# Performance work log

Hardware: AMD Instinct MI355X
Metric: run time of the kernel (lower is better)

Reference implementation:

```python
import jax, jax.numpy as jnp
import numpy as np

E, H, L = 512, 512, 1   # emb_size, hidden_size, num_layers
B, S, T = 64, 1024, 256  # batch, src_len, trg_len
SCALE = 0.02


def setup_inputs() -> dict:
    key = jax.random.key(0)
    ks = jax.random.split(key, 12)
    f32 = jnp.float32
    return {
        # forward args
        "trg_embed": jax.random.normal(ks[0], (B, T, E), f32),
        "encoder_hidden": jax.random.normal(ks[1], (B, S, 2 * H), f32),
        "encoder_final": jax.random.normal(ks[2], (L, B, 2 * H), f32),
        "src_mask": jnp.ones((B, 1, S), jnp.bool_),
        "trg_mask": jnp.ones((B, 1, T), jnp.bool_),
        # Bahdanau attention params
        "W_key": jax.random.normal(ks[3], (H, 2 * H), f32) * SCALE,
        "W_query": jax.random.normal(ks[4], (H, H), f32) * SCALE,
        "v_energy": jax.random.normal(ks[5], (H,), f32) * SCALE,
        # bridge (2H -> H, with bias)
        "W_bridge": jax.random.normal(ks[6], (H, 2 * H), f32) * SCALE,
        "b_bridge": jnp.zeros((H,), f32),
        # GRU (single layer), gate order r,z,n as in torch
        "W_ih": jax.random.normal(ks[7], (3 * H, E + 2 * H), f32) * SCALE,
        "W_hh": jax.random.normal(ks[8], (3 * H, H), f32) * SCALE,
        "b_ih": jnp.zeros((3 * H,), f32),
        "b_hh": jnp.zeros((3 * H,), f32),
        # pre_output_layer: (H + 2H + E) -> H, no bias
        "W_pre": jax.random.normal(ks[9], (H, H + 2 * H + E), f32) * SCALE,
    }


def _gru_cell(x, h, W_ih, W_hh, b_ih, b_hh):
    # x: [B, E+2H], h: [B, H]; torch GRUCell math, gates r,z,n
    gi = x @ W_ih.T + b_ih
    gh = h @ W_hh.T + b_hh
    i_r, i_z, i_n = jnp.split(gi, 3, axis=-1)
    h_r, h_z, h_n = jnp.split(gh, 3, axis=-1)
    r = jax.nn.sigmoid(i_r + h_r)
    z = jax.nn.sigmoid(i_z + h_z)
    n = jnp.tanh(i_n + r * h_n)
    return (1.0 - z) * n + z * h


def reference(trg_embed, encoder_hidden, encoder_final, src_mask, trg_mask,
              W_key, W_query, v_energy, W_bridge, b_bridge,
              W_ih, W_hh, b_ih, b_hh, W_pre):
    # init_hidden: tanh(bridge(encoder_final))  -> [L, B, H]
    hidden0 = jnp.tanh(jnp.einsum('lbd,hd->lbh', encoder_final, W_bridge) + b_bridge)
    # precomputed attention keys: [B, S, H]
    proj_key = jnp.einsum('bsd,hd->bsh', encoder_hidden, W_key)
    mask = src_mask[:, 0, :]  # [B, S]
    neg = jnp.finfo(trg_embed.dtype).min

    def step(hidden, prev_embed):  # hidden [L,B,H], prev_embed [B,E]
        q = hidden[-1] @ W_query.T                       # [B, H]
        e = jnp.tanh(q[:, None, :] + proj_key)           # [B, S, H]
        scores = jnp.einsum('bsh,h->bs', e, v_energy)    # [B, S]
        scores = jnp.where(mask, scores, neg)
        alphas = jax.nn.softmax(scores, axis=-1)         # [B, S]
        context = jnp.einsum('bs,bsd->bd', alphas, encoder_hidden)  # [B, 2H]
        x = jnp.concatenate([prev_embed, context], axis=-1)         # [B, E+2H]
        h_new = _gru_cell(x, hidden[-1], W_ih, W_hh, b_ih, b_hh)    # [B, H]
        pre = jnp.concatenate([prev_embed, h_new, context], axis=-1) @ W_pre.T  # [B, H]
        return h_new[None, :, :], (h_new, pre)

    hidden_final, (outs, pres) = jax.lax.scan(step, hidden0, jnp.swapaxes(trg_embed, 0, 1))
    decoder_states = jnp.swapaxes(outs, 0, 1)        # [B, T, H]
    pre_output_vectors = jnp.swapaxes(pres, 0, 1)    # [B, T, H]
    return decoder_states, hidden_final, pre_output_vectors
```

## Files before the change

### kernel.cpp

```cpp
#include <hip/hip_runtime.h>


typedef __attribute__((ext_vector_type(8))) short bf16x8;
typedef __attribute__((ext_vector_type(4))) float f32x4;
typedef __attribute__((ext_vector_type(2))) float f32x2;
typedef unsigned short u16;
typedef unsigned char u8;
typedef unsigned int u32;

constexpr int NB = 64, NS = 1024, NT = 256, NE = 512, NH = 512, NH2 = 1024, NG3 = 1536;

#define MFMA16(a, b, c) __builtin_amdgcn_mfma_f32_16x16x32_bf16((a), (b), (c), 0, 0, 0)

__device__ __forceinline__ float bf2f(u16 u) { return __uint_as_float(((u32)u) << 16); }
__device__ __forceinline__ u16 f2bf(float f) {
    u32 u = __float_as_uint(f);
    u += 0x7FFFu + ((u >> 16) & 1u);
    return (u16)(u >> 16);
}
__device__ __forceinline__ float fast_tanh(float x) {
    float t = __expf(2.0f * x);
    return 1.0f - __fdividef(2.0f, t + 1.0f);
}
__device__ __forceinline__ float fast_sig(float x) {
    return __fdividef(1.0f, 1.0f + __expf(-x));
}

__global__ void k_cast(const float* __restrict__ src, u16* __restrict__ dst, int n4) {
    int i = blockIdx.x * blockDim.x + threadIdx.x;
    int stride = gridDim.x * blockDim.x;
    for (; i < n4; i += stride) {
        float4 v = reinterpret_cast<const float4*>(src)[i];
        ushort4 o;
        o.x = f2bf(v.x); o.y = f2bf(v.y); o.z = f2bf(v.z); o.w = f2bf(v.w);
        reinterpret_cast<ushort4*>(dst)[i] = o;
    }
}
__global__ void k_cast8(const float* __restrict__ src, u32* __restrict__ dst, int n8) {
    int i = blockIdx.x * blockDim.x + threadIdx.x;
    int stride = gridDim.x * blockDim.x;
    for (; i < n8; i += stride) {
        float4 a = reinterpret_cast<const float4*>(src)[i * 2];
        float4 b = reinterpret_cast<const float4*>(src)[i * 2 + 1];
        int w0 = 0, w1 = 0;
        w0 = __builtin_amdgcn_cvt_pk_fp8_f32(a.x, a.y, w0, false);
        w0 = __builtin_amdgcn_cvt_pk_fp8_f32(a.z, a.w, w0, true);
        w1 = __builtin_amdgcn_cvt_pk_fp8_f32(b.x, b.y, w1, false);
        w1 = __builtin_amdgcn_cvt_pk_fp8_f32(b.z, b.w, w1, true);
        uint2 o; o.x = (u32)w0; o.y = (u32)w1;
        reinterpret_cast<uint2*>(dst)[i] = o;
    }
}

__global__ __launch_bounds__(256) void k_pkgemm8(
    const float* __restrict__ A, const u16* __restrict__ Bm, u8* __restrict__ Out8) {
    __shared__ u16 As[128][72];
    __shared__ u16 Bs[128][72];
    const int mt = blockIdx.x, nt = blockIdx.y;
    const int tid = threadIdx.x, lane = tid & 63, wv = tid >> 6;
    const int m0 = mt * 128, n0 = nt * 128;
    const f32x4 fz = {0.f, 0.f, 0.f, 0.f};
    f32x4 acc[2][8];
#pragma unroll
    for (int i = 0; i < 2; ++i)
#pragma unroll
        for (int jj = 0; jj < 8; ++jj) acc[i][jj] = fz;

    for (int kt = 0; kt < 16; ++kt) {
        const int k0 = kt * 64;
        __syncthreads();
#pragma unroll
        for (int r = 0; r < 4; ++r) {
            int cc = tid + 256 * r;
            int row = cc >> 3, kc = (cc & 7) * 8;
            const float* ap = &A[(size_t)(m0 + row) * NH2 + k0 + kc];
            float4 f0 = *(const float4*)ap;
            float4 f1 = *(const float4*)(ap + 4);
            u16 hh[8] = {f2bf(f0.x), f2bf(f0.y), f2bf(f0.z), f2bf(f0.w),
                         f2bf(f1.x), f2bf(f1.y), f2bf(f1.z), f2bf(f1.w)};
            *(bf16x8*)&As[row][kc] = *(bf16x8*)hh;
            *(bf16x8*)&Bs[row][kc] = *(const bf16x8*)&Bm[(size_t)(n0 + row) * NH2 + k0 + kc];
        }
        __syncthreads();
#pragma unroll
        for (int ks = 0; ks < 2; ++ks) {
            const int kk = ks * 32 + (lane >> 4) * 8;
            bf16x8 a0 = *(const bf16x8*)&As[wv * 32 + (lane & 15)][kk];
            bf16x8 a1 = *(const bf16x8*)&As[wv * 32 + 16 + (lane & 15)][kk];
#pragma unroll
            for (int jj = 0; jj < 8; ++jj) {
                bf16x8 bb = *(const bf16x8*)&Bs[jj * 16 + (lane & 15)][kk];
                acc[0][jj] = MFMA16(a0, bb, acc[0][jj]);
                acc[1][jj] = MFMA16(a1, bb, acc[1][jj]);
            }
        }
    }
#pragma unroll
    for (int i = 0; i < 2; ++i)
#pragma unroll
        for (int jj = 0; jj < 8; ++jj)
#pragma unroll
            for (int r = 0; r < 4; ++r) {
                int m = m0 + wv * 32 + i * 16 + (lane >> 4) * 4 + r;
                int n = n0 + jj * 16 + (lane & 15);
                int pk = __builtin_amdgcn_cvt_pk_fp8_f32(acc[i][jj][r], acc[i][jj][r], 0, false);
                Out8[(size_t)m * NH + n] = (u8)(pk & 0xFF);
            }
}

__global__ __launch_bounds__(256) void k_bridge(
    const float* __restrict__ ef, const float* __restrict__ Wb, const float* __restrict__ bb,
    float* __restrict__ hf, u16* __restrict__ hbb) {
    __shared__ float efs[NH2];
    const int b = blockIdx.x, tid = threadIdx.x;
    for (int i = tid; i < NH2; i += 256) efs[i] = ef[(size_t)b * NH2 + i];
    __syncthreads();
    for (int j = tid; j < NH; j += 256) {
        float acc = bb[j];
        const float4* wr = (const float4*)&Wb[(size_t)j * NH2];
#pragma unroll 4
        for (int d4 = 0; d4 < 256; ++d4) {
            float4 w = wr[d4];
            acc += w.x * efs[d4 * 4] + w.y * efs[d4 * 4 + 1] + w.z * efs[d4 * 4 + 2] + w.w * efs[d4 * 4 + 3];
        }
        float h0 = tanhf(acc);
        hf[(size_t)b * NH + j] = h0;
        hbb[(size_t)b * NH + j] = f2bf(h0);
    }
}

__global__ __launch_bounds__(256, 4) void k_attn(
    const u8* __restrict__ pk8, const u8* __restrict__ eh8,
    const float* __restrict__ qb, const float* __restrict__ ven,
    u16* __restrict__ ctxp, float* __restrict__ denp) {
    __shared__ float wts[64];
    __shared__ float wden[4];
    __shared__ float part[64][4][17];
    const int b = blockIdx.x >> 4, c = blockIdx.x & 15;
    const int tid = threadIdx.x, lane = tid & 63, wv = tid >> 6;
    const int sl = lane & 3, ch = lane >> 2;
    const int h0 = ch * 32;
    const float C = 2.8853900817779268f;
    float qv2[32], vvm2[32];
    float vs = 0.f;
#pragma unroll
    for (int i4 = 0; i4 < 8; ++i4) {
        float4 q4 = *(const float4*)&qb[(size_t)b * NH + h0 + i4 * 4];
        float4 v4 = *(const float4*)&ven[h0 + i4 * 4];
        qv2[i4 * 4 + 0] = C * q4.x; qv2[i4 * 4 + 1] = C * q4.y;
        qv2[i4 * 4 + 2] = C * q4.z; qv2[i4 * 4 + 3] = C * q4.w;
        vvm2[i4 * 4 + 0] = -2.f * v4.x; vvm2[i4 * 4 + 1] = -2.f * v4.y;
        vvm2[i4 * 4 + 2] = -2.f * v4.z; vvm2[i4 * 4 + 3] = -2.f * v4.w;
        vs += v4.x + v4.y + v4.z + v4.w;
    }
#pragma unroll
    for (int off = 32; off; off >>= 1) vs += __shfl_xor(vs, off, 64);
    vs *= 0.25f;

    const u8* pkbase = pk8 + ((size_t)b * NS + c * 64 + wv * 16 + sl) * NH + h0;
    u32 pk[4][8];
#pragma unroll
    for (int g = 0; g < 4; ++g) {
        const u8* row = pkbase + (size_t)g * 4 * NH;
        *(uint4*)&pk[g][0] = *(const uint4*)row;
        *(uint4*)&pk[g][4] = *(const uint4*)(row + 16);
    }
    float accg[4];
#pragma unroll
    for (int g = 0; g < 4; ++g) {
        float acc0 = 0.f, acc1 = 0.f;
#pragma unroll
        for (int w = 0; w < 8; ++w) {
            f32x2 lo = __builtin_amdgcn_cvt_pk_f32_fp8(pk[g][w], false);
            f32x2 hi = __builtin_amdgcn_cvt_pk_f32_fp8(pk[g][w], true);
            const int i = w * 4;
            float x0 = __builtin_fmaf(lo[0], C, qv2[i + 0]);
            float x1 = __builtin_fmaf(lo[1], C, qv2[i + 1]);
            float x2 = __builtin_fmaf(hi[0], C, qv2[i + 2]);
            float x3 = __builtin_fmaf(hi[1], C, qv2[i + 3]);
            acc0 = __builtin_fmaf(vvm2[i + 0], __builtin_amdgcn_rcpf(__builtin_amdgcn_exp2f(x0) + 1.0f), acc0);
            acc1 = __builtin_fmaf(vvm2[i + 1], __builtin_amdgcn_rcpf(__builtin_amdgcn_exp2f(x1) + 1.0f), acc1);
            acc0 = __builtin_fmaf(vvm2[i + 2], __builtin_amdgcn_rcpf(__builtin_amdgcn_exp2f(x2) + 1.0f), acc0);
            acc1 = __builtin_fmaf(vvm2[i + 3], __builtin_amdgcn_rcpf(__builtin_amdgcn_exp2f(x3) + 1.0f), acc1);
        }
        accg[g] = acc0 + acc1;
    }
#pragma unroll
    for (int off = 4; off <= 32; off <<= 1) {
#pragma unroll
        for (int g = 0; g < 4; ++g) accg[g] += __shfl_xor(accg[g], off, 64);
    }
    float den_acc = 0.f;
#pragma unroll
    for (int g = 0; g < 4; ++g) {
        float w = __expf(accg[g] + vs);
        if (lane < 4) wts[wv * 16 + g * 4 + lane] = w;
        den_acc += w;
    }
#pragma unroll
    for (int off = 32; off; off >>= 1) den_acc += __shfl_xor(den_acc, off, 64);
    if (lane == 0) wden[wv] = den_acc * 0.0625f;

    const int qd = wv, tt = lane;
    const int d0 = tt * 16;
    const u8* ebase = eh8 + ((size_t)b * NS + c * 64 + qd * 16) * NH2 + d0;
    float ar[16];
#pragma unroll
    for (int k = 0; k < 16; ++k) ar[k] = 0.f;
#pragma unroll 4
    for (int s = 0; s < 16; ++s) {
        float w = wts[qd * 16 + s];
        uint4 uu = *(const uint4*)&ebase[(size_t)s * NH2];
        const u32 ww[4] = {uu.x, uu.y, uu.z, uu.w};
#pragma unroll
        for (int q = 0; q < 4; ++q) {
            f32x2 plo = __builtin_amdgcn_cvt_pk_f32_fp8(ww[q], false);
            f32x2 phi = __builtin_amdgcn_cvt_pk_f32_fp8(ww[q], true);
            ar[q * 4 + 0] = __builtin_fmaf(w, plo[0], ar[q * 4 + 0]);
            ar[q * 4 + 1] = __builtin_fmaf(w, plo[1], ar[q * 4 + 1]);
            ar[q * 4 + 2] = __builtin_fmaf(w, phi[0], ar[q * 4 + 2]);
            ar[q * 4 + 3] = __builtin_fmaf(w, phi[1], ar[q * 4 + 3]);
        }
    }
#pragma unroll
    for (int k = 0; k < 16; ++k) part[tt][qd][k] = ar[k];
    __syncthreads();
    if (tid == 0) denp[c * 64 + b] = wden[0] + wden[1] + wden[2] + wden[3];
    const int st = tid >> 2, k0 = (tid & 3) * 4;
    float o0 = 0.f, o1 = 0.f, o2 = 0.f, o3 = 0.f;
#pragma unroll
    for (int q = 0; q < 4; ++q) {
        o0 += part[st][q][k0 + 0];
        o1 += part[st][q][k0 + 1];
        o2 += part[st][q][k0 + 2];
        o3 += part[st][q][k0 + 3];
    }
    ushort4 o;
    o.x = f2bf(o0); o.y = f2bf(o1); o.z = f2bf(o2); o.w = f2bf(o3);
    *(ushort4*)&ctxp[((size_t)c * 64 + b) * NH2 + tid * 4] = o;
}

__global__ __launch_bounds__(256) void k_norm(
    const u16* __restrict__ ctxp, const float* __restrict__ denp,
    u16* __restrict__ ctxb, u16* __restrict__ ctxall, int t) {
    const int b = blockIdx.x >> 1, half = blockIdx.x & 1;
    const int tid = threadIdx.x;
    float den = 0.f;
#pragma unroll
    for (int c = 0; c < 16; ++c) den += denp[c * 64 + b];
    float rd = 1.0f / den;
    const int d0 = half * 512 + tid * 2;
    float ax = 0.f, ay = 0.f;
#pragma unroll
    for (int c = 0; c < 16; ++c) {
        ushort2 v = *(const ushort2*)&ctxp[((size_t)c * 64 + b) * NH2 + d0];
        ax += bf2f(v.x); ay += bf2f(v.y);
    }
    ushort2 o;
    o.x = f2bf(ax * rd); o.y = f2bf(ay * rd);
    *(ushort2*)&ctxb[(size_t)b * NH2 + d0] = o;
    *(ushort2*)&ctxall[((size_t)b * NT + t) * NH2 + d0] = o;
}

__global__ __launch_bounds__(512) void k_gru(
    const u16* __restrict__ teb, const u16* __restrict__ ctxb, const u16* __restrict__ hb_in,
    const u16* __restrict__ Wihb, const u16* __restrict__ Whhb,
    const float* __restrict__ bih, const float* __restrict__ bhh,
    const float* __restrict__ hf_in, float* __restrict__ hf_out, u16* __restrict__ hb_out,
    u16* __restrict__ hall, float* __restrict__ out_ds, float* __restrict__ out_hf, int t) {
    __shared__ float pbuf[3][7][16][17];
    const int tid = threadIdx.x, lane = tid & 63, wv = tid >> 6;
    const int g = blockIdx.x;
    const int jt = g & 31, mh = g >> 5;
    const int jj = lane & 15;
    const int j = jt * 16 + jj;
    const int kg = lane >> 4;
    const int mrow = mh * 8 + (jj & 7);

    const f32x4 fz = {0.f, 0.f, 0.f, 0.f};
    f32x4 g0 = fz, g1 = fz, g2 = fz;
    const u16* wr = Wihb + (size_t)j * NG3;
    const u16* wz = wr + (size_t)NH * NG3;
    const u16* wn = wr + (size_t)NH2 * NG3;
    float ho[4], bset[6];

    if (wv < 2) {
        const u16* ta = teb + ((size_t)mrow * NT + t) * NE;
#pragma unroll
        for (int kt = 0; kt < 8; ++kt) {
            int k0 = (wv * 8 + kt) * 32 + kg * 8;
            bf16x8 a = *(const bf16x8*)&ta[k0];
            g0 = MFMA16(a, *(const bf16x8*)&wr[k0], g0);
            g1 = MFMA16(a, *(const bf16x8*)&wz[k0], g1);
            g2 = MFMA16(a, *(const bf16x8*)&wn[k0], g2);
        }
        if (wv == 0) {
            bset[0] = bih[j]; bset[1] = bih[NH + j]; bset[2] = bih[NH2 + j];
            bset[3] = bhh[j]; bset[4] = bhh[NH + j]; bset[5] = bhh[NH2 + j];
#pragma unroll
            for (int r = 0; r < 4; ++r) {
                int ml = kg * 4 + r;
                ho[r] = (ml < 8) ? hf_in[(size_t)(mh * 8 + ml) * NH + j] : 0.f;
            }
        }
    } else if (wv < 4) {
        const u16* ha = hb_in + (size_t)mrow * NH;
        const u16* vr = Whhb + (size_t)j * NH;
        const u16* vz = vr + (size_t)NH * NH;
        const u16* vn = vr + (size_t)NH2 * NH;
#pragma unroll
        for (int kt = 0; kt < 8; ++kt) {
            int k0 = ((wv - 2) * 8 + kt) * 32 + kg * 8;
            bf16x8 a = *(const bf16x8*)&ha[k0];
            g0 = MFMA16(a, *(const bf16x8*)&vr[k0], g0);
            g1 = MFMA16(a, *(const bf16x8*)&vz[k0], g1);
            g2 = MFMA16(a, *(const bf16x8*)&vn[k0], g2);
        }
    } else {
        const int koff = (wv - 4) * 256;
        const u16* ca = ctxb + (size_t)mrow * NH2;
#pragma unroll
        for (int kt = 0; kt < 8; ++kt) {
            int kc = koff + kt * 32 + kg * 8;
            bf16x8 a = *(const bf16x8*)&ca[kc];
            g0 = MFMA16(a, *(const bf16x8*)&wr[NE + kc], g0);
            g1 = MFMA16(a, *(const bf16x8*)&wz[NE + kc], g1);
            g2 = MFMA16(a, *(const bf16x8*)&wn[NE + kc], g2);
        }
    }
    if (wv != 0) {
        const int src = wv - 1;
#pragma unroll
        for (int r = 0; r < 4; ++r) {
            int ml = kg * 4 + r;
            pbuf[0][src][ml][jj] = g0[r];
            pbuf[1][src][ml][jj] = g1[r];
            pbuf[2][src][ml][jj] = g2[r];
        }
    }
    __syncthreads();

    if (wv == 0) {
#pragma unroll
        for (int r = 0; r < 4; ++r) {
            int ml = kg * 4 + r;
            if (ml >= 8) continue;
            int m = mh * 8 + ml;
            float gir = g0[r] + pbuf[0][0][ml][jj] + pbuf[0][3][ml][jj] + pbuf[0][4][ml][jj]
                      + pbuf[0][5][ml][jj] + pbuf[0][6][ml][jj] + bset[0];
            float giz = g1[r] + pbuf[1][0][ml][jj] + pbuf[1][3][ml][jj] + pbuf[1][4][ml][jj]
                      + pbuf[1][5][ml][jj] + pbuf[1][6][ml][jj] + bset[1];
            float gin = g2[r] + pbuf[2][0][ml][jj] + pbuf[2][3][ml][jj] + pbuf[2][4][ml][jj]
                      + pbuf[2][5][ml][jj] + pbuf[2][6][ml][jj] + bset[2];
            float ghr = pbuf[0][1][ml][jj] + pbuf[0][2][ml][jj] + bset[3];
            float ghz = pbuf[1][1][ml][jj] + pbuf[1][2][ml][jj] + bset[4];
            float ghn = pbuf[2][1][ml][jj] + pbuf[2][2][ml][jj] + bset[5];
            float rr = fast_sig(gir + ghr);
            float zz = fast_sig(giz + ghz);
            float nn = fast_tanh(gin + rr * ghn);
            float hn = (1.f - zz) * nn + zz * ho[r];
            u16 hb = f2bf(hn);
            hf_out[(size_t)m * NH + j] = hn;
            hb_out[(size_t)m * NH + j] = hb;
            hall[((size_t)m * NT + t) * NH + j] = hb;
            __builtin_nontemporal_store(hn, &out_ds[((size_t)m * NT + t) * NH + j]);
            if (t == NT - 1) out_hf[(size_t)m * NH + j] = hn;
        }
    }
}

__global__ __launch_bounds__(512) void k_q(
    const u16* __restrict__ hbn, const u16* __restrict__ Wqb, float* __restrict__ qbuf) {
    __shared__ float qp[64][17];
    const int tid = threadIdx.x, lane = tid & 63, wv = tid >> 6;
    const int wv4 = wv & 3, khalf = wv >> 2;
    const int mrow = wv4 * 16 + (lane & 15);
    const int kg = lane >> 4;
    const int n = blockIdx.x * 16 + (lane & 15);
    const f32x4 fz = {0.f, 0.f, 0.f, 0.f};
    f32x4 aq = fz;
    const u16* ha = hbn + (size_t)mrow * NH;
    const u16* wq = Wqb + (size_t)n * NH;
#pragma unroll
    for (int kt = 0; kt < 8; ++kt) {
        int k0 = (khalf * 8 + kt) * 32 + kg * 8;
        aq = MFMA16(*(const bf16x8*)&ha[k0], *(const bf16x8*)&wq[k0], aq);
    }
    if (khalf == 1) {
#pragma unroll
        for (int r = 0; r < 4; ++r) {
            int m = wv4 * 16 + kg * 4 + r;
            qp[m][lane & 15] = aq[r];
        }
    }
    __syncthreads();
    if (khalf == 0) {
#pragma unroll
        for (int r = 0; r < 4; ++r) {
            int m = wv4 * 16 + kg * 4 + r;
            qbuf[(size_t)m * NH + n] = aq[r] + qp[m][lane & 15];
        }
    }
}

__global__ __launch_bounds__(256) void k_preb(
    const u16* __restrict__ teb, const u16* __restrict__ hall, const u16* __restrict__ ctxall,
    const u16* __restrict__ Wpreb, float* __restrict__ out_pre) {
    __shared__ u16 As[128][72];
    __shared__ u16 Bs[128][72];
    const int mt = blockIdx.x, nt = blockIdx.y;
    const int tid = threadIdx.x, lane = tid & 63, wv = tid >> 6;
    const int m0 = mt * 128, n0 = nt * 128;
    const f32x4 fz = {0.f, 0.f, 0.f, 0.f};
    f32x4 acc[2][8];
#pragma unroll
    for (int i = 0; i < 2; ++i)
#pragma unroll
        for (int jj = 0; jj < 8; ++jj) acc[i][jj] = fz;

    for (int kt = 0; kt < 32; ++kt) {
        const int k0 = kt * 64;
        const u16* Abase; int astride, acol;
        if (k0 < 512)       { Abase = teb;    astride = 512;  acol = k0; }
        else if (k0 < 1024) { Abase = hall;   astride = 512;  acol = k0 - 512; }
        else                { Abase = ctxall; astride = 1024; acol = k0 - 1024; }
        __syncthreads();
#pragma unroll
        for (int r = 0; r < 4; ++r) {
            int cc = tid + 256 * r;
            int row = cc >> 3, kc = (cc & 7) * 8;
            *(bf16x8*)&As[row][kc] = *(const bf16x8*)&Abase[(size_t)(m0 + row) * astride + acol + kc];
            *(bf16x8*)&Bs[row][kc] = *(const bf16x8*)&Wpreb[(size_t)(n0 + row) * 2048 + k0 + kc];
        }
        __syncthreads();
#pragma unroll
        for (int ks = 0; ks < 2; ++ks) {
            const int kk = ks * 32 + (lane >> 4) * 8;
            bf16x8 a0 = *(const bf16x8*)&As[wv * 32 + (lane & 15)][kk];
            bf16x8 a1 = *(const bf16x8*)&As[wv * 32 + 16 + (lane & 15)][kk];
#pragma unroll
            for (int jj = 0; jj < 8; ++jj) {
                bf16x8 bb = *(const bf16x8*)&Bs[jj * 16 + (lane & 15)][kk];
                acc[0][jj] = MFMA16(a0, bb, acc[0][jj]);
                acc[1][jj] = MFMA16(a1, bb, acc[1][jj]);
            }
        }
    }
#pragma unroll
    for (int i = 0; i < 2; ++i)
#pragma unroll
        for (int jj = 0; jj < 8; ++jj)
#pragma unroll
            for (int r = 0; r < 4; ++r) {
                int m = m0 + wv * 32 + i * 16 + (lane >> 4) * 4 + r;
                int n = n0 + jj * 16 + (lane & 15);
                __builtin_nontemporal_store(acc[i][jj][r], &out_pre[(size_t)m * NH + n]);
            }
}

extern "C" void kernel_launch(void* const* d_in, const int* in_sizes, int n_in,
                              void* d_out, int out_size, void* d_ws, size_t ws_size,
                              hipStream_t stream) {
    const float* trg_embed  = (const float*)d_in[0];
    const float* enc_hidden = (const float*)d_in[1];
    const float* enc_final  = (const float*)d_in[2];
    const float* W_key    = (const float*)d_in[5];
    const float* W_query  = (const float*)d_in[6];
    const float* v_energy = (const float*)d_in[7];
    const float* W_bridge = (const float*)d_in[8];
    const float* b_bridge = (const float*)d_in[9];
    const float* W_ih     = (const float*)d_in[10];
    const float* W_hh     = (const float*)d_in[11];
    const float* b_ih     = (const float*)d_in[12];
    const float* b_hh     = (const float*)d_in[13];
    const float* W_pre    = (const float*)d_in[14];

    if (ws_size < 180000000ULL) return;
    size_t off = 0;
    auto take = [&](size_t bytes) {
        void* p = (char*)d_ws + off;
        off += (bytes + 255) & ~(size_t)255;
        return p;
    };
    u8*    eh8   = (u8*)take((size_t)NB * NS * NH2);
    u8*    pk8   = (u8*)take((size_t)NB * NS * NH);
    u16*   teb   = (u16*)take((size_t)NB * NT * NE * 2);
    u16*   ctxall= (u16*)take((size_t)NB * NT * NH2 * 2);
    u16*   hall  = (u16*)take((size_t)NB * NT * NH * 2);
    u16*   Wihb  = (u16*)take((size_t)NG3 * NG3 * 2);
    u16*   Whhb  = (u16*)take((size_t)NG3 * NH * 2);
    u16*   Wpreb = (u16*)take((size_t)NH * 2048 * 2);
    u16*   Wqb   = (u16*)take((size_t)NH * NH * 2);
    u16*   Wkb   = (u16*)take((size_t)NH * NH2 * 2);
    float* hf0   = (float*)take((size_t)NB * NH * 4);
    float* hf1   = (float*)take((size_t)NB * NH * 4);
    u16*   hb0   = (u16*)take((size_t)NB * NH * 2);
    u16*   hb1   = (u16*)take((size_t)NB * NH * 2);
    float* qbuf  = (float*)take((size_t)NB * NH * 4);
    u16*   ctxp  = (u16*)take((size_t)16 * NB * NH2 * 2);
    float* denp  = (float*)take((size_t)16 * NB * 4);
    u16*   ctxb  = (u16*)take((size_t)NB * NH2 * 2);

    float* out_ds  = (float*)d_out;
    float* out_hf  = out_ds + (size_t)NB * NT * NH;
    float* out_pre = out_hf + (size_t)NB * NH;

    auto cast = [&](const float* src, u16* dst, int n) {
        int n4 = n / 4;
        int grid = (n4 + 255) / 256; if (grid > 2048) grid = 2048;
        k_cast<<<grid, 256, 0, stream>>>(src, dst, n4);
    };
    k_cast8<<<2048, 256, 0, stream>>>(enc_hidden, (u32*)eh8, NB * NS * NH2 / 8);
    cast(trg_embed,  teb, NB * NT * NE);
    cast(W_ih,  Wihb,  NG3 * NG3);
    cast(W_hh,  Whhb,  NG3 * NH);
    cast(W_pre, Wpreb, NH * 2048);
    cast(W_query, Wqb, NH * NH);
    cast(W_key,  Wkb,  NH * NH2);
    k_pkgemm8<<<dim3(512, 4), 256, 0, stream>>>(enc_hidden, Wkb, pk8);
    k_bridge<<<NB, 256, 0, stream>>>(enc_final, W_bridge, b_bridge, hf0, hb0);
    k_q<<<32, 512, 0, stream>>>(hb0, Wqb, qbuf);

    for (int t = 0; t < NT; ++t) {
        float* hf_in  = (t & 1) ? hf1 : hf0;
        float* hf_out = (t & 1) ? hf0 : hf1;
        u16*   hb_in  = (t & 1) ? hb1 : hb0;
        u16*   hb_out = (t & 1) ? hb0 : hb1;
        k_attn<<<NB * 16, 256, 0, stream>>>(pk8, eh8, qbuf, v_energy, ctxp, denp);
        k_norm<<<NB * 2, 256, 0, stream>>>(ctxp, denp, ctxb, ctxall, t);
        k_gru<<<256, 512, 0, stream>>>(teb, ctxb, hb_in, Wihb, Whhb, b_ih, b_hh,
                                       hf_in, hf_out, hb_out, hall,
                                       out_ds, out_hf, t);
        k_q<<<32, 512, 0, stream>>>(hb_out, Wqb, qbuf);
    }
    k_preb<<<dim3(128, 4), 256, 0, stream>>>(teb, hall, ctxall, Wpreb, out_pre);
}
```

Measured before the change: 9.419 ms.

## Move hidden-state GEMM out of GRU kernel into fused query kernel

The h@W_hh product now runs in the query-projection kernel of the previous step and is stored to a global gate buffer, so the GRU kernel only does the input and context GEMMs, spread evenly over all 8 waves. This takes the recurrent matmul off the critical path of the GRU launch at the cost of a larger k_qg grid and an extra fp32 buffer round-trip. Separately, the attention context loop now preloads all 16 fp8 rows into registers before accumulating, which exposes more memory-level parallelism but raises register pressure.

```diff
diff --git a/kernel.cpp b/kernel.cpp
--- a/kernel.cpp
+++ b/kernel.cpp
@@ -204,14 +204,16 @@
     const int qd = wv, tt = lane;
     const int d0 = tt * 16;
     const u8* ebase = eh8 + ((size_t)b * NS + c * 64 + qd * 16) * NH2 + d0;
+    uint4 uu[16];
+#pragma unroll
+    for (int s = 0; s < 16; ++s) uu[s] = *(const uint4*)&ebase[(size_t)s * NH2];
     float ar[16];
 #pragma unroll
     for (int k = 0; k < 16; ++k) ar[k] = 0.f;
-#pragma unroll 4
+#pragma unroll
     for (int s = 0; s < 16; ++s) {
         float w = wts[qd * 16 + s];
-        uint4 uu = *(const uint4*)&ebase[(size_t)s * NH2];
-        const u32 ww[4] = {uu.x, uu.y, uu.z, uu.w};
+        const u32 ww[4] = {uu[s].x, uu[s].y, uu[s].z, uu[s].w};
 #pragma unroll
         for (int q = 0; q < 4; ++q) {
             f32x2 plo = __builtin_amdgcn_cvt_pk_f32_fp8(ww[q], false);
@@ -263,8 +265,8 @@
 }
 
 __global__ __launch_bounds__(512) void k_gru(
-    const u16* __restrict__ teb, const u16* __restrict__ ctxb, const u16* __restrict__ hb_in,
-    const u16* __restrict__ Wihb, const u16* __restrict__ Whhb,
+    const u16* __restrict__ teb, const u16* __restrict__ ctxb,
+    const u16* __restrict__ Wihb, const float* __restrict__ ghb,
     const float* __restrict__ bih, const float* __restrict__ bhh,
     const float* __restrict__ hf_in, float* __restrict__ hf_out, u16* __restrict__ hb_out,
     u16* __restrict__ hall, float* __restrict__ out_ds, float* __restrict__ out_hf, int t) {
@@ -282,53 +284,41 @@
     const u16* wr = Wihb + (size_t)j * NG3;
     const u16* wz = wr + (size_t)NH * NG3;
     const u16* wn = wr + (size_t)NH2 * NG3;
-    float ho[4], bset[6];
-
-    if (wv < 2) {
-        const u16* ta = teb + ((size_t)mrow * NT + t) * NE;
-#pragma unroll
-        for (int kt = 0; kt < 8; ++kt) {
-            int k0 = (wv * 8 + kt) * 32 + kg * 8;
+    const u16* ta = teb + ((size_t)mrow * NT + t) * NE;
+    const u16* ca = ctxb + (size_t)mrow * NH2;
+    float ho[4], bset[6], ghv[3][4];
+
+    const int vk0 = wv * 6;
+#pragma unroll
+    for (int i = 0; i < 6; ++i) {
+        const int vk = vk0 + i;
+        if (vk < 16) {
+            int k0 = vk * 32 + kg * 8;
             bf16x8 a = *(const bf16x8*)&ta[k0];
             g0 = MFMA16(a, *(const bf16x8*)&wr[k0], g0);
             g1 = MFMA16(a, *(const bf16x8*)&wz[k0], g1);
             g2 = MFMA16(a, *(const bf16x8*)&wn[k0], g2);
-        }
-        if (wv == 0) {
-            bset[0] = bih[j]; bset[1] = bih[NH + j]; bset[2] = bih[NH2 + j];
-            bset[3] = bhh[j]; bset[4] = bhh[NH + j]; bset[5] = bhh[NH2 + j];
-#pragma unroll
-            for (int r = 0; r < 4; ++r) {
-                int ml = kg * 4 + r;
-                ho[r] = (ml < 8) ? hf_in[(size_t)(mh * 8 + ml) * NH + j] : 0.f;
-            }
-        }
-    } else if (wv < 4) {
-        const u16* ha = hb_in + (size_t)mrow * NH;
-        const u16* vr = Whhb + (size_t)j * NH;
-        const u16* vz = vr + (size_t)NH * NH;
-        const u16* vn = vr + (size_t)NH2 * NH;
-#pragma unroll
-        for (int kt = 0; kt < 8; ++kt) {
-            int k0 = ((wv - 2) * 8 + kt) * 32 + kg * 8;
-            bf16x8 a = *(const bf16x8*)&ha[k0];
-            g0 = MFMA16(a, *(const bf16x8*)&vr[k0], g0);
-            g1 = MFMA16(a, *(const bf16x8*)&vz[k0], g1);
-            g2 = MFMA16(a, *(const bf16x8*)&vn[k0], g2);
-        }
-    } else {
-        const int koff = (wv - 4) * 256;
-        const u16* ca = ctxb + (size_t)mrow * NH2;
-#pragma unroll
-        for (int kt = 0; kt < 8; ++kt) {
-            int kc = koff + kt * 32 + kg * 8;
+        } else {
+            int kc = (vk - 16) * 32 + kg * 8;
             bf16x8 a = *(const bf16x8*)&ca[kc];
             g0 = MFMA16(a, *(const bf16x8*)&wr[NE + kc], g0);
             g1 = MFMA16(a, *(const bf16x8*)&wz[NE + kc], g1);
             g2 = MFMA16(a, *(const bf16x8*)&wn[NE + kc], g2);
         }
     }
-    if (wv != 0) {
+    if (wv == 0) {
+        bset[0] = bih[j]; bset[1] = bih[NH + j]; bset[2] = bih[NH2 + j];
+        bset[3] = bhh[j]; bset[4] = bhh[NH + j]; bset[5] = bhh[NH2 + j];
+#pragma unroll
+        for (int r = 0; r < 4; ++r) {
+            int ml = kg * 4 + r;
+            int m = mh * 8 + (ml & 7);
+            ho[r] = (ml < 8) ? hf_in[(size_t)m * NH + j] : 0.f;
+#pragma unroll
+            for (int gg = 0; gg < 3; ++gg)
+                ghv[gg][r] = (ml < 8) ? ghb[(size_t)m * NG3 + gg * NH + j] : 0.f;
+        }
+    } else {
         const int src = wv - 1;
 #pragma unroll
         for (int r = 0; r < 4; ++r) {
@@ -346,18 +336,17 @@
             int ml = kg * 4 + r;
             if (ml >= 8) continue;
             int m = mh * 8 + ml;
-            float gir = g0[r] + pbuf[0][0][ml][jj] + pbuf[0][3][ml][jj] + pbuf[0][4][ml][jj]
-                      + pbuf[0][5][ml][jj] + pbuf[0][6][ml][jj] + bset[0];
-            float giz = g1[r] + pbuf[1][0][ml][jj] + pbuf[1][3][ml][jj] + pbuf[1][4][ml][jj]
-                      + pbuf[1][5][ml][jj] + pbuf[1][6][ml][jj] + bset[1];
-            float gin = g2[r] + pbuf[2][0][ml][jj] + pbuf[2][3][ml][jj] + pbuf[2][4][ml][jj]
-                      + pbuf[2][5][ml][jj] + pbuf[2][6][ml][jj] + bset[2];
-            float ghr = pbuf[0][1][ml][jj] + pbuf[0][2][ml][jj] + bset[3];
-            float ghz = pbuf[1][1][ml][jj] + pbuf[1][2][ml][jj] + bset[4];
-            float ghn = pbuf[2][1][ml][jj] + pbuf[2][2][ml][jj] + bset[5];
-            float rr = fast_sig(gir + ghr);
-            float zz = fast_sig(giz + ghz);
-            float nn = fast_tanh(gin + rr * ghn);
+            float gir = g0[r], giz = g1[r], gin = g2[r];
+#pragma unroll
+            for (int src = 0; src < 7; ++src) {
+                gir += pbuf[0][src][ml][jj];
+                giz += pbuf[1][src][ml][jj];
+                gin += pbuf[2][src][ml][jj];
+            }
+            gir += bset[0]; giz += bset[1]; gin += bset[2];
+            float rr = fast_sig(gir + ghv[0][r] + bset[3]);
+            float zz = fast_sig(giz + ghv[1][r] + bset[4]);
+            float nn = fast_tanh(gin + rr * (ghv[2][r] + bset[5]));
             float hn = (1.f - zz) * nn + zz * ho[r];
             u16 hb = f2bf(hn);
             hf_out[(size_t)m * NH + j] = hn;
@@ -369,28 +358,32 @@
     }
 }
 
-__global__ __launch_bounds__(512) void k_q(
-    const u16* __restrict__ hbn, const u16* __restrict__ Wqb, float* __restrict__ qbuf) {
+__global__ __launch_bounds__(512) void k_qg(
+    const u16* __restrict__ hbn, const u16* __restrict__ Wqb, const u16* __restrict__ Whhb,
+    float* __restrict__ qbuf, float* __restrict__ ghb) {
     __shared__ float qp[64][17];
     const int tid = threadIdx.x, lane = tid & 63, wv = tid >> 6;
     const int wv4 = wv & 3, khalf = wv >> 2;
     const int mrow = wv4 * 16 + (lane & 15);
     const int kg = lane >> 4;
-    const int n = blockIdx.x * 16 + (lane & 15);
+    const int nt = blockIdx.x;
+    const int nloc = (lane & 15);
+    const bool isq = (nt < 32);
+    const u16* brow = isq ? (Wqb + (size_t)(nt * 16 + nloc) * NH)
+                          : (Whhb + (size_t)((nt - 32) * 16 + nloc) * NH);
     const f32x4 fz = {0.f, 0.f, 0.f, 0.f};
     f32x4 aq = fz;
     const u16* ha = hbn + (size_t)mrow * NH;
-    const u16* wq = Wqb + (size_t)n * NH;
 #pragma unroll
     for (int kt = 0; kt < 8; ++kt) {
         int k0 = (khalf * 8 + kt) * 32 + kg * 8;
-        aq = MFMA16(*(const bf16x8*)&ha[k0], *(const bf16x8*)&wq[k0], aq);
+        aq = MFMA16(*(const bf16x8*)&ha[k0], *(const bf16x8*)&brow[k0], aq);
     }
     if (khalf == 1) {
 #pragma unroll
         for (int r = 0; r < 4; ++r) {
             int m = wv4 * 16 + kg * 4 + r;
-            qp[m][lane & 15] = aq[r];
+            qp[m][nloc] = aq[r];
         }
     }
     __syncthreads();
@@ -398,7 +391,9 @@
 #pragma unroll
         for (int r = 0; r < 4; ++r) {
             int m = wv4 * 16 + kg * 4 + r;
-            qbuf[(size_t)m * NH + n] = aq[r] + qp[m][lane & 15];
+            float v = aq[r] + qp[m][nloc];
+            if (isq) qbuf[(size_t)m * NH + nt * 16 + nloc] = v;
+            else     ghb[(size_t)m * NG3 + (nt - 32) * 16 + nloc] = v;
         }
     }
 }
@@ -497,6 +492,7 @@
     u16*   hb0   = (u16*)take((size_t)NB * NH * 2);
     u16*   hb1   = (u16*)take((size_t)NB * NH * 2);
     float* qbuf  = (float*)take((size_t)NB * NH * 4);
+    float* ghb   = (float*)take((size_t)NB * NG3 * 4);
     u16*   ctxp  = (u16*)take((size_t)16 * NB * NH2 * 2);
     float* denp  = (float*)take((size_t)16 * NB * 4);
     u16*   ctxb  = (u16*)take((size_t)NB * NH2 * 2);
@@ -519,19 +515,18 @@
     cast(W_key,  Wkb,  NH * NH2);
     k_pkgemm8<<<dim3(512, 4), 256, 0, stream>>>(enc_hidden, Wkb, pk8);
     k_bridge<<<NB, 256, 0, stream>>>(enc_final, W_bridge, b_bridge, hf0, hb0);
-    k_q<<<32, 512, 0, stream>>>(hb0, Wqb, qbuf);
+    k_qg<<<128, 512, 0, stream>>>(hb0, Wqb, Whhb, qbuf, ghb);
 
     for (int t = 0; t < NT; ++t) {
         float* hf_in  = (t & 1) ? hf1 : hf0;
         float* hf_out = (t & 1) ? hf0 : hf1;
-        u16*   hb_in  = (t & 1) ? hb1 : hb0;
         u16*   hb_out = (t & 1) ? hb0 : hb1;
         k_attn<<<NB * 16, 256, 0, stream>>>(pk8, eh8, qbuf, v_energy, ctxp, denp);
         k_norm<<<NB * 2, 256, 0, stream>>>(ctxp, denp, ctxb, ctxall, t);
-        k_gru<<<256, 512, 0, stream>>>(teb, ctxb, hb_in, Wihb, Whhb, b_ih, b_hh,
+        k_gru<<<256, 512, 0, stream>>>(teb, ctxb, Wihb, ghb, b_ih, b_hh,
                                        hf_in, hf_out, hb_out, hall,
                                        out_ds, out_hf, t);
-        k_q<<<32, 512, 0, stream>>>(hb_out, Wqb, qbuf);
+        k_qg<<<128, 512, 0, stream>>>(hb_out, Wqb, Whhb, qbuf, ghb);
     }
     k_preb<<<dim3(128, 4), 256, 0, stream>>>(teb, hall, ctxall, Wpreb, out_pre);
 }
```

Result: slower. 18.00 ms (+91.1%).
